# Performance work log

Hardware: AMD Instinct MI355X
Metric: run time of the kernel (lower is better)

Reference implementation:

```python
import jax, jax.numpy as jnp
import numpy as np

N_NODES = 50000
N_EDGES = 300000
HIDDEN = 256
Z_DIM = 128
N_LAYERS = 3
NUM_GRAPHS = 16
EPS = 1e-5


def setup_inputs() -> dict:
    key = jax.random.key(0)
    ks = jax.random.split(key, 16)
    s = 0.05
    inp = {
        "voxel_pos": jax.random.normal(ks[0], (N_NODES, 3), jnp.float32),
        "edge_index": jax.random.randint(ks[1], (2, N_EDGES), 0, N_NODES),
        "batch_index": jnp.sort(jax.random.randint(ks[2], (N_NODES,), 0, NUM_GRAPHS)),
        # input projection Linear(3, H) + GroupNorm(1, H) affine
        "W_in": jax.random.normal(ks[3], (3, HIDDEN), jnp.float32) * s,
        "b_in": jnp.zeros((HIDDEN,), jnp.float32),
        "g_in": jnp.ones((HIDDEN,), jnp.float32),
        "be_in": jnp.zeros((HIDDEN,), jnp.float32),
        # stacked GCNConv weights/biases and per-layer GroupNorm affines
        "conv_W": jax.random.normal(ks[4], (N_LAYERS, HIDDEN, HIDDEN), jnp.float32) * s,
        "conv_b": jnp.zeros((N_LAYERS, HIDDEN), jnp.float32),
        "gn_g": jnp.ones((N_LAYERS, HIDDEN), jnp.float32),
        "gn_b": jnp.zeros((N_LAYERS, HIDDEN), jnp.float32),
        # output MLP: Linear(H,H) -> ReLU -> GroupNorm -> Linear(H, Z)
        "W_o1": jax.random.normal(ks[5], (HIDDEN, HIDDEN), jnp.float32) * s,
        "b_o1": jnp.zeros((HIDDEN,), jnp.float32),
        "g_o": jnp.ones((HIDDEN,), jnp.float32),
        "be_o": jnp.zeros((HIDDEN,), jnp.float32),
        "W_o2": jax.random.normal(ks[6], (HIDDEN, Z_DIM), jnp.float32) * s,
        "b_o2": jnp.zeros((Z_DIM,), jnp.float32),
    }
    return inp


def group_norm(x, g, b):
    # GroupNorm(1, C) on (N, C): normalize over channels per node (biased var)
    mu = jnp.mean(x, axis=-1, keepdims=True)
    var = jnp.mean(jnp.square(x - mu), axis=-1, keepdims=True)
    return (x - mu) * jax.lax.rsqrt(var + EPS) * g + b


def reference(voxel_pos, edge_index, batch_index, W_in, b_in, g_in, be_in,
              conv_W, conv_b, gn_g, gn_b, W_o1, b_o1, g_o, be_o, W_o2, b_o2):
    n = voxel_pos.shape[0]
    loop = jnp.arange(n, dtype=edge_index.dtype)
    src = jnp.concatenate([edge_index[0], loop])  # A + I self-loops (PyG GCNConv default)
    dst = jnp.concatenate([edge_index[1], loop])
    deg = jax.ops.segment_sum(jnp.ones_like(dst, jnp.float32), dst, num_segments=n)
    dinv = jnp.where(deg > 0, jax.lax.rsqrt(jnp.maximum(deg, 1.0)), 0.0)
    enorm = dinv[src] * dinv[dst]  # D^{-1/2} (A+I) D^{-1/2} edge weights

    # input_proj: Linear -> ReLU -> GroupNorm
    x = group_norm(jax.nn.relu(voxel_pos @ W_in + b_in), g_in, be_in)

    for l in range(N_LAYERS):
        identity = x
        h = x @ conv_W[l]                      # GCNConv linear transform
        msg = h[src] * enorm[:, None]          # gather + scale (E+N, H)
        h = jax.ops.segment_sum(msg, dst, num_segments=n) + conv_b[l]
        x = jax.nn.relu(group_norm(h, gn_g[l], gn_b[l])) + identity

    # global mean pool per graph
    summed = jax.ops.segment_sum(x, batch_index, num_segments=NUM_GRAPHS)
    counts = jax.ops.segment_sum(jnp.ones((n,), jnp.float32), batch_index, num_segments=NUM_GRAPHS)
    pooled = summed / jnp.maximum(counts, 1.0)[:, None]

    h = group_norm(jax.nn.relu(pooled @ W_o1 + b_o1), g_o, be_o)
    return h @ W_o2 + b_o2
```

## Files before the change

### kernel.cpp

```cpp
#include <hip/hip_runtime.h>
#include <hip/hip_bf16.h>

#define N_NODES 50000
#define N_EDGES 300000
#define HIDDEN 256
#define ZDIM 128
#define NLAYERS 3
#define NGRAPHS 16
#define EPS 1e-5f
#define NSCANBLK 196

#define OFF_POS    0
#define OFF_WIN    150000
#define OFF_BIN    150768
#define OFF_GIN    151024
#define OFF_BEIN   151280
#define OFF_CONVB  348144
#define OFF_GNG    348912
#define OFF_GNB    349680
#define OFF_WO1    350448
#define OFF_BO1    415984
#define OFF_GO     416240
#define OFF_BEO    416496
#define OFF_WO2    416752
#define OFF_BO2    449520
#define PARAMS_TOTAL 449648

typedef __attribute__((ext_vector_type(8))) short short8;
typedef __attribute__((ext_vector_type(4))) float floatx4;

__device__ inline float wave_reduce_sum(float v){
#pragma unroll
  for (int off = 32; off; off >>= 1) v += __shfl_xor(v, off);
  return v;
}

__device__ inline ushort f2bf(float f){
  __hip_bfloat16 t = __float2bfloat16(f);
  return *(ushort*)&t;
}
__device__ inline float bflo(unsigned int u){ return __uint_as_float(u << 16); }
__device__ inline float bfhi(unsigned int u){ return __uint_as_float(u & 0xffff0000u); }

__device__ inline void gload_lds16(const void* g, void* l){
  __builtin_amdgcn_global_load_lds((const __attribute__((address_space(1))) void*)g,
                                   (__attribute__((address_space(3))) void*)l, 16, 0, 0);
}

__device__ inline void acc8(float* a, float w, uint4 v){
  a[0] = fmaf(w, bflo(v.x), a[0]); a[1] = fmaf(w, bfhi(v.x), a[1]);
  a[2] = fmaf(w, bflo(v.y), a[2]); a[3] = fmaf(w, bfhi(v.y), a[3]);
  a[4] = fmaf(w, bflo(v.z), a[4]); a[5] = fmaf(w, bfhi(v.z), a[5]);
  a[6] = fmaf(w, bflo(v.w), a[6]); a[7] = fmaf(w, bfhi(v.w), a[7]);
}

struct PrepArgs { const void* src[14]; int n[14]; int off[14]; const void* win; const void* convw; };

__global__ __launch_bounds__(256) void k_prep(PrepArgs a, float* __restrict__ params,
                                              ushort* __restrict__ Wt, int* __restrict__ flag,
                                              int* __restrict__ deg, int* __restrict__ fill,
                                              float* __restrict__ pooled, float* __restrict__ counts){
  __shared__ int sf;
  int tid = threadIdx.x;
  if (tid == 0) sf = 0;
  __syncthreads();
  const unsigned short* w = (const unsigned short*)a.win;
  for (int i = tid; i < 768; i += 256){
    int e = (w[i] >> 7) & 0xff;
    if (e >= 148) atomicOr(&sf, 1);
  }
  __syncthreads();
  const bool isf32 = (sf != 0);
  if (blockIdx.x == 0 && tid == 0) *flag = sf;

  int stride = gridDim.x * blockDim.x;
  int t0 = blockIdx.x * blockDim.x + tid;
  for (int i = t0; i < N_NODES; i += stride){ deg[i] = 1; fill[i] = 0; }
  for (int i = t0; i < NGRAPHS * 256; i += stride) pooled[i] = 0.f;
  for (int i = t0; i < NGRAPHS; i += stride) counts[i] = 0.f;

  for (int s = 0; s < 14; ++s){
    const void* src = a.src[s];
    int n = a.n[s];
    float* dst = params + a.off[s];
    if (isf32){
      const float* f = (const float*)src;
      for (int i = t0; i < n; i += stride) dst[i] = f[i];
    } else {
      const unsigned short* u = (const unsigned short*)src;
      for (int i = t0; i < n; i += stride) dst[i] = bflo(u[i]);
    }
  }
  for (int idx = t0; idx < NLAYERS * 65536; idx += stride){
    int l = idx >> 16, rem = idx & 65535, n = rem >> 8, k = rem & 255;
    int si = l * 65536 + k * 256 + n;
    float v = isf32 ? ((const float*)a.convw)[si] : bflo(((const unsigned short*)a.convw)[si]);
    Wt[idx] = f2bf(v);
  }
}

__global__ void k_deg(const int* __restrict__ dst, int* __restrict__ deg){
  int e = blockIdx.x * blockDim.x + threadIdx.x;
  if (e < N_EDGES) atomicAdd(&deg[dst[e]], 1);
}

__global__ __launch_bounds__(256) void k_scan1(const int* __restrict__ deg, int* __restrict__ row_start,
                                               int* __restrict__ bsum, float* __restrict__ dinv){
  __shared__ int sd[256];
  int tid = threadIdx.x;
  int i = blockIdx.x * 256 + tid;
  int v = (i < N_NODES) ? deg[i] : 0;
  if (i < N_NODES) dinv[i] = rsqrtf((float)v);
  sd[tid] = v;
  __syncthreads();
#pragma unroll
  for (int off = 1; off < 256; off <<= 1){
    int t = (tid >= off) ? sd[tid - off] : 0;
    __syncthreads();
    sd[tid] += t;
    __syncthreads();
  }
  if (i < N_NODES) row_start[i] = sd[tid];
  if (tid == 255) bsum[blockIdx.x] = sd[255];
}

__global__ __launch_bounds__(256) void k_scan2(const int* __restrict__ bsum, int* __restrict__ boff,
                                               int* __restrict__ row_start){
  __shared__ int sd[256];
  int tid = threadIdx.x;
  int v = (tid < NSCANBLK) ? bsum[tid] : 0;
  sd[tid] = v;
  __syncthreads();
#pragma unroll
  for (int off = 1; off < 256; off <<= 1){
    int t = (tid >= off) ? sd[tid - off] : 0;
    __syncthreads();
    sd[tid] += t;
    __syncthreads();
  }
  if (tid < NSCANBLK) boff[tid] = sd[tid] - v;
  if (tid == NSCANBLK - 1) row_start[N_NODES] = sd[tid];
}

__global__ __launch_bounds__(256) void k_scan3(const int* __restrict__ deg, const int* __restrict__ boff,
                                               int* __restrict__ row_start){
  int i = blockIdx.x * 256 + threadIdx.x;
  if (i < N_NODES) row_start[i] = row_start[i] + boff[blockIdx.x] - deg[i];
}

__global__ void k_fill(const int* __restrict__ src, const int* __restrict__ dst,
                       const int* __restrict__ row_start, int* __restrict__ fill,
                       const float* __restrict__ dinv, uint2* __restrict__ csr){
  int t = blockIdx.x * blockDim.x + threadIdx.x;
  if (t >= N_EDGES + N_NODES) return;
  int s, d;
  if (t < N_EDGES){ s = src[t]; d = dst[t]; }
  else            { s = t - N_EDGES; d = s; }
  int pos = row_start[d] + atomicAdd(&fill[d], 1);
  uint2 e; e.x = (unsigned)s; e.y = __float_as_uint(dinv[s] * dinv[d]);
  csr[pos] = e;
}

__global__ __launch_bounds__(256) void k_input_proj(const float* __restrict__ params,
                                                    ushort* __restrict__ x_bf){
  int lane = threadIdx.x & 63;
  int node = (blockIdx.x << 2) + (threadIdx.x >> 6);
  if (node >= N_NODES) return;
  const float* pos = params + OFF_POS + node * 3;
  float px = pos[0], py = pos[1], pz = pos[2];
  int c = lane * 4;
  const float* w0 = params + OFF_WIN;
  float v[4];
#pragma unroll
  for (int j = 0; j < 4; ++j){
    float t = params[OFF_BIN + c + j];
    t = fmaf(px, w0[c + j], t);
    t = fmaf(py, w0[256 + c + j], t);
    t = fmaf(pz, w0[512 + c + j], t);
    v[j] = fmaxf(t, 0.f);
  }
  float s  = v[0] + v[1] + v[2] + v[3];
  float ss = v[0]*v[0] + v[1]*v[1] + v[2]*v[2] + v[3]*v[3];
  s = wave_reduce_sum(s); ss = wave_reduce_sum(ss);
  float mean = s * (1.f/256.f);
  float var  = ss * (1.f/256.f) - mean * mean;
  float inv  = rsqrtf(var + EPS);
  float4 o;
  o.x = (v[0]-mean)*inv*params[OFF_GIN+c+0] + params[OFF_BEIN+c+0];
  o.y = (v[1]-mean)*inv*params[OFF_GIN+c+1] + params[OFF_BEIN+c+1];
  o.z = (v[2]-mean)*inv*params[OFF_GIN+c+2] + params[OFF_BEIN+c+2];
  o.w = (v[3]-mean)*inv*params[OFF_GIN+c+3] + params[OFF_BEIN+c+3];
  ushort4 ob = { f2bf(o.x), f2bf(o.y), f2bf(o.z), f2bf(o.w) };
  *(ushort4*)(x_bf + node * 256 + c) = ob;
}

#define GBM 128
__global__ __launch_bounds__(256) void k_gemm_bf(const ushort* __restrict__ A, const ushort* __restrict__ Bt,
                                                 ushort* __restrict__ Cb, int M){
  __shared__ __align__(16) ushort Sh[2 * GBM * 64];
  ushort* As = Sh;
  ushort* Bs = Sh + GBM * 64;
  int tid = threadIdx.x;
  int wave = tid >> 6, lane = tid & 63;
  int wr = wave >> 1, wc = wave & 1;
  int row0 = blockIdx.y * GBM;
  int col0 = blockIdx.x * GBM;
  int q = lane >> 4, l15 = lane & 15;
  int srow = lane >> 3;
  int sg   = lane & 7;
  floatx4 acc[4][4] = {};
  for (int k0 = 0; k0 < 256; k0 += 64){
    __syncthreads();
#pragma unroll
    for (int t = 0; t < 4; ++t){
      int rg = wave * 4 + t;
      int r  = rg * 8 + srow;
      int gs = sg ^ (r & 7);
      const ushort* ga = A  + (size_t)(row0 + r) * 256 + k0 + gs * 8;
      const ushort* gb = Bt + (size_t)(col0 + r) * 256 + k0 + gs * 8;
      gload_lds16(ga, As + rg * 512);
      gload_lds16(gb, Bs + rg * 512);
    }
    __syncthreads();
#pragma unroll
    for (int kk = 0; kk < 64; kk += 32){
      short8 af[4], bfr[4];
#pragma unroll
      for (int i = 0; i < 4; ++i){
        int R = wr * 64 + i * 16 + l15;
        int bg = (kk >> 3) + q;
        af[i] = *(const short8*)(As + R * 64 + ((bg ^ (R & 7)) << 3));
      }
#pragma unroll
      for (int j = 0; j < 4; ++j){
        int C = wc * 64 + j * 16 + l15;
        int bg = (kk >> 3) + q;
        bfr[j] = *(const short8*)(Bs + C * 64 + ((bg ^ (C & 7)) << 3));
      }
#pragma unroll
      for (int i = 0; i < 4; ++i)
#pragma unroll
        for (int j = 0; j < 4; ++j)
          acc[i][j] = __builtin_amdgcn_mfma_f32_16x16x32_bf16(af[i], bfr[j], acc[i][j], 0, 0, 0);
    }
  }
#pragma unroll
  for (int i = 0; i < 4; ++i){
#pragma unroll
    for (int r = 0; r < 4; ++r){
      int row = row0 + wr * 64 + i * 16 + q * 4 + r;
      if (row < M){
#pragma unroll
        for (int j = 0; j < 4; ++j){
          int col = col0 + wc * 64 + j * 16 + l15;
          Cb[row * 256 + col] = f2bf(acc[i][j][r]);
        }
      }
    }
  }
}

__global__ __launch_bounds__(256) void k_agg_norm(const ushort* __restrict__ hb, ushort* __restrict__ x_bf,
    const int* __restrict__ row_start, const uint2* __restrict__ csr,
    const float* __restrict__ params, int layer){
  int lane = threadIdx.x & 63;
  int node = (blockIdx.x << 2) + (threadIdx.x >> 6);
  if (node >= N_NODES) return;
  int half = lane >> 5;
  int l32 = lane & 31;
  int c = l32 * 8;
  float a[8] = {};
  int p0 = row_start[node], p1 = row_start[node + 1];
  int p = p0;
  for (; p + 8 <= p1; p += 8){
    uint2 e0 = csr[p + 0 + half];
    uint2 e1 = csr[p + 2 + half];
    uint2 e2 = csr[p + 4 + half];
    uint2 e3 = csr[p + 6 + half];
    uint4 v0 = *(const uint4*)(hb + (size_t)e0.x * 256 + c);
    uint4 v1 = *(const uint4*)(hb + (size_t)e1.x * 256 + c);
    uint4 v2 = *(const uint4*)(hb + (size_t)e2.x * 256 + c);
    uint4 v3 = *(const uint4*)(hb + (size_t)e3.x * 256 + c);
    acc8(a, __uint_as_float(e0.y), v0);
    acc8(a, __uint_as_float(e1.y), v1);
    acc8(a, __uint_as_float(e2.y), v2);
    acc8(a, __uint_as_float(e3.y), v3);
  }
  for (; p < p1; p += 2){
    int pp = p + half;
    if (pp < p1){
      uint2 e = csr[pp];
      uint4 v = *(const uint4*)(hb + (size_t)e.x * 256 + c);
      acc8(a, __uint_as_float(e.y), v);
    }
  }
#pragma unroll
  for (int j = 0; j < 8; ++j) a[j] += __shfl_xor(a[j], 32);

  const float* cb = params + OFF_CONVB + layer * 256;
  float v8[8];
  float s = 0.f, ss = 0.f;
#pragma unroll
  for (int j = 0; j < 8; ++j){
    float t = a[j] + cb[c + j];
    v8[j] = t; s += t; ss += t * t;
  }
  s  = wave_reduce_sum(s)  * 0.5f;
  ss = wave_reduce_sum(ss) * 0.5f;
  float mean = s * (1.f/256.f);
  float var  = ss * (1.f/256.f) - mean * mean;
  float inv  = rsqrtf(var + EPS);
  if (half == 0){
    const float* g = params + OFF_GNG + layer * 256;
    const float* b = params + OFF_GNB + layer * 256;
    uint4 xo = *(const uint4*)(x_bf + (size_t)node * 256 + c);
    float xr[8] = { bflo(xo.x), bfhi(xo.x), bflo(xo.y), bfhi(xo.y),
                    bflo(xo.z), bfhi(xo.z), bflo(xo.w), bfhi(xo.w) };
    short8 ob;
#pragma unroll
    for (int j = 0; j < 8; ++j){
      float o = fmaxf((v8[j] - mean) * inv * g[c + j] + b[c + j], 0.f) + xr[j];
      ob[j] = (short)f2bf(o);
    }
    *(short8*)(x_bf + (size_t)node * 256 + c) = ob;
  }
}

#define PBLK 256
__global__ __launch_bounds__(256) void k_pool(const ushort* __restrict__ x_bf, const int* __restrict__ batch,
                                              float* __restrict__ pooled, float* __restrict__ counts){
  __shared__ float lacc[NGRAPHS][256];
  __shared__ float lcnt[NGRAPHS];
  int tid = threadIdx.x;
  int wave = tid >> 6, lane = tid & 63;
  int c = lane * 4;
#pragma unroll
  for (int g = 0; g < NGRAPHS; ++g) lacc[g][tid] = 0.f;
  if (tid < NGRAPHS) lcnt[tid] = 0.f;
  __syncthreads();

  int n0 = blockIdx.x * PBLK + wave * 64;
  if (n0 < N_NODES){
    int n1 = min(n0 + 64, N_NODES);
    int b0 = batch[n0], b1 = batch[n1 - 1];
    float a0 = 0.f, a1 = 0.f, a2 = 0.f, a3 = 0.f;
    if (b0 == b1){
      int i = n0;
      for (; i + 8 <= n1; i += 8){
        uint2 v[8];
#pragma unroll
        for (int j = 0; j < 8; ++j) v[j] = *(const uint2*)(x_bf + (size_t)(i + j) * 256 + c);
#pragma unroll
        for (int j = 0; j < 8; ++j){
          a0 += bflo(v[j].x); a1 += bfhi(v[j].x);
          a2 += bflo(v[j].y); a3 += bfhi(v[j].y);
        }
      }
      for (; i < n1; ++i){
        uint2 v = *(const uint2*)(x_bf + (size_t)i * 256 + c);
        a0 += bflo(v.x); a1 += bfhi(v.x); a2 += bflo(v.y); a3 += bfhi(v.y);
      }
      atomicAdd(&lacc[b0][c + 0], a0); atomicAdd(&lacc[b0][c + 1], a1);
      atomicAdd(&lacc[b0][c + 2], a2); atomicAdd(&lacc[b0][c + 3], a3);
      if (lane == 0) atomicAdd(&lcnt[b0], (float)(n1 - n0));
    } else {
      int cur = b0, cnt = 0;
      for (int i = n0; i < n1; ++i){
        int g = batch[i];
        if (g != cur){
          atomicAdd(&lacc[cur][c + 0], a0); atomicAdd(&lacc[cur][c + 1], a1);
          atomicAdd(&lacc[cur][c + 2], a2); atomicAdd(&lacc[cur][c + 3], a3);
          if (lane == 0) atomicAdd(&lcnt[cur], (float)cnt);
          a0 = a1 = a2 = a3 = 0.f; cnt = 0; cur = g;
        }
        uint2 v = *(const uint2*)(x_bf + (size_t)i * 256 + c);
        a0 += bflo(v.x); a1 += bfhi(v.x); a2 += bflo(v.y); a3 += bfhi(v.y);
        cnt++;
      }
      atomicAdd(&lacc[cur][c + 0], a0); atomicAdd(&lacc[cur][c + 1], a1);
      atomicAdd(&lacc[cur][c + 2], a2); atomicAdd(&lacc[cur][c + 3], a3);
      if (lane == 0) atomicAdd(&lcnt[cur], (float)cnt);
    }
  }
  __syncthreads();

  int base = blockIdx.x * PBLK;
  if (base < N_NODES){
    int gmin = batch[base];
    int gmax = batch[min(base + PBLK, N_NODES) - 1];
    for (int g = gmin; g <= gmax; ++g){
      float v = lacc[g][tid];
      if (v != 0.f) atomicAdd(&pooled[g * 256 + tid], v);
      if (tid == 0 && lcnt[g] > 0.f) atomicAdd(&counts[g], lcnt[g]);
    }
  }
}

__global__ __launch_bounds__(256) void k_head(const float* __restrict__ pooled, const float* __restrict__ counts,
    const float* __restrict__ params, void* __restrict__ out, const int* __restrict__ flag){
  __shared__ float m[256];
  __shared__ float hh[256];
  __shared__ float red[2][4];
  int g = blockIdx.x, tid = threadIdx.x;
  float cnt = fmaxf(counts[g], 1.f);
  m[tid] = pooled[g * 256 + tid] / cnt;
  __syncthreads();
  const float* W1 = params + OFF_WO1;
  float acc = params[OFF_BO1 + tid];
  for (int k = 0; k < 256; ++k) acc = fmaf(m[k], W1[k * 256 + tid], acc);
  acc = fmaxf(acc, 0.f);
  float s = wave_reduce_sum(acc), ss = wave_reduce_sum(acc * acc);
  int wv = tid >> 6, lane = tid & 63;
  if (lane == 0){ red[0][wv] = s; red[1][wv] = ss; }
  __syncthreads();
  float S  = red[0][0] + red[0][1] + red[0][2] + red[0][3];
  float SS = red[1][0] + red[1][1] + red[1][2] + red[1][3];
  float mean = S * (1.f/256.f);
  float var  = SS * (1.f/256.f) - mean * mean;
  float inv  = rsqrtf(var + EPS);
  float hn = (acc - mean) * inv * params[OFF_GO + tid] + params[OFF_BEO + tid];
  hh[tid] = hn;
  __syncthreads();
  if (tid < ZDIM){
    const float* W2 = params + OFF_WO2;
    float o = params[OFF_BO2 + tid];
    for (int k = 0; k < 256; ++k) o = fmaf(hh[k], W2[k * 128 + tid], o);
    if (*flag) ((float*)out)[g * 128 + tid] = o;
    else       ((__hip_bfloat16*)out)[g * 128 + tid] = __float2bfloat16(o);
  }
}

extern "C" void kernel_launch(void* const* d_in, const int* in_sizes, int n_in,
                              void* d_out, int out_size, void* d_ws, size_t ws_size,
                              hipStream_t stream){
  size_t o = 0;
  auto alloc = [&](size_t bytes)->size_t{ size_t r = o; o = (o + bytes + 255) & ~(size_t)255; return r; };
  size_t off_flag   = alloc(4);
  size_t off_deg    = alloc((size_t)N_NODES * 4);
  size_t off_dinv   = alloc((size_t)N_NODES * 4);
  size_t off_rs     = alloc((size_t)(N_NODES + 1) * 4);
  size_t off_fill   = alloc((size_t)N_NODES * 4);
  size_t off_bsum   = alloc((size_t)NSCANBLK * 4);
  size_t off_boff   = alloc((size_t)NSCANBLK * 4);
  size_t off_csr    = alloc((size_t)(N_EDGES + N_NODES) * 8);
  size_t off_params = alloc((size_t)PARAMS_TOTAL * 4);
  size_t off_xbf    = alloc((size_t)N_NODES * HIDDEN * 2);
  size_t off_hbf    = alloc((size_t)N_NODES * HIDDEN * 2);
  size_t off_wt     = alloc((size_t)NLAYERS * HIDDEN * HIDDEN * 2);
  size_t off_pool   = alloc((size_t)NGRAPHS * 256 * 4);
  size_t off_cnt    = alloc((size_t)NGRAPHS * 4);
  if (o > ws_size) return;

  char* ws = (char*)d_ws;
  int*    flag     = (int*)(ws + off_flag);
  int*    deg      = (int*)(ws + off_deg);
  float*  dinv     = (float*)(ws + off_dinv);
  int*    row_start= (int*)(ws + off_rs);
  int*    fill     = (int*)(ws + off_fill);
  int*    bsum     = (int*)(ws + off_bsum);
  int*    boff     = (int*)(ws + off_boff);
  uint2*  csr      = (uint2*)(ws + off_csr);
  float*  params   = (float*)(ws + off_params);
  ushort* x_bf     = (ushort*)(ws + off_xbf);
  ushort* h_bf     = (ushort*)(ws + off_hbf);
  ushort* Wt       = (ushort*)(ws + off_wt);
  float*  pooled   = (float*)(ws + off_pool);
  float*  counts   = (float*)(ws + off_cnt);

  const int* edge_src = (const int*)d_in[1];
  const int* edge_dst = (const int*)d_in[1] + N_EDGES;
  const int* batch    = (const int*)d_in[2];

  PrepArgs pa;
  const int srcIdx[14] = {0,3,4,5,6,8,9,10,11,12,13,14,15,16};
  const int ns[14]     = {150000,768,256,256,256,768,768,768,65536,256,256,256,32768,128};
  const int offs[14]   = {OFF_POS,OFF_WIN,OFF_BIN,OFF_GIN,OFF_BEIN,OFF_CONVB,OFF_GNG,OFF_GNB,
                          OFF_WO1,OFF_BO1,OFF_GO,OFF_BEO,OFF_WO2,OFF_BO2};
  for (int i = 0; i < 14; ++i){ pa.src[i] = d_in[srcIdx[i]]; pa.n[i] = ns[i]; pa.off[i] = offs[i]; }
  pa.win = d_in[3]; pa.convw = d_in[7];
  k_prep<<<512, 256, 0, stream>>>(pa, params, Wt, flag, deg, fill, pooled, counts);

  k_deg<<<(N_EDGES + 255) / 256, 256, 0, stream>>>(edge_dst, deg);
  k_scan1<<<NSCANBLK, 256, 0, stream>>>(deg, row_start, bsum, dinv);
  k_scan2<<<1, 256, 0, stream>>>(bsum, boff, row_start);
  k_scan3<<<NSCANBLK, 256, 0, stream>>>(deg, boff, row_start);
  k_fill<<<(N_EDGES + N_NODES + 255) / 256, 256, 0, stream>>>(edge_src, edge_dst, row_start, fill,
                                                              dinv, csr);
  k_input_proj<<<N_NODES / 4, 256, 0, stream>>>(params, x_bf);

  dim3 ggrid(2, (N_NODES + GBM - 1) / GBM);
  for (int l = 0; l < NLAYERS; ++l){
    k_gemm_bf<<<ggrid, 256, 0, stream>>>(x_bf, Wt + l * 65536, h_bf, N_NODES);
    k_agg_norm<<<N_NODES / 4, 256, 0, stream>>>(h_bf, x_bf, row_start, csr, params, l);
  }

  k_pool<<<(N_NODES + PBLK - 1) / PBLK, 256, 0, stream>>>(x_bf, batch, pooled, counts);
  k_head<<<NGRAPHS, 256, 0, stream>>>(pooled, counts, params, d_out, flag);
}
```

Measured before the change: 350.8 us.

## Fuse scan fixup, CSR fill and input projection; tile weight transpose via LDS

After: 345.4 us. About the same (-1.5%).

```diff
diff --git a/kernel.cpp b/kernel.cpp
--- a/kernel.cpp
+++ b/kernel.cpp
@@ -9,6 +9,7 @@
 #define NGRAPHS 16
 #define EPS 1e-5f
 #define NSCANBLK 196
+#define FILLB 1368
 
 #define OFF_POS    0
 #define OFF_WIN    150000
@@ -61,6 +62,7 @@
                                               int* __restrict__ deg, int* __restrict__ fill,
                                               float* __restrict__ pooled, float* __restrict__ counts){
   __shared__ int sf;
+  __shared__ ushort tile[64][72];
   int tid = threadIdx.x;
   if (tid == 0) sf = 0;
   __syncthreads();
@@ -72,6 +74,28 @@
   __syncthreads();
   const bool isf32 = (sf != 0);
   if (blockIdx.x == 0 && tid == 0) *flag = sf;
+
+  if (blockIdx.x < NLAYERS * 16){
+    int t = blockIdx.x;
+    int l = t >> 4, tt = t & 15;
+    int kr0 = (tt >> 2) * 64, nc0 = (tt & 3) * 64;
+    size_t base = (size_t)l * 65536;
+    int r = tid >> 2;
+    int seg = (tid & 3) * 16;
+    if (isf32){
+      const float* srcp = (const float*)a.convw + base + (size_t)(kr0 + r) * 256 + nc0 + seg;
+#pragma unroll
+      for (int j = 0; j < 16; ++j) tile[r][seg + j] = f2bf(srcp[j]);
+    } else {
+      const unsigned short* srcp = (const unsigned short*)a.convw + base + (size_t)(kr0 + r) * 256 + nc0 + seg;
+#pragma unroll
+      for (int j = 0; j < 16; ++j) tile[r][seg + j] = srcp[j];
+    }
+    __syncthreads();
+    ushort* dst = Wt + base + (size_t)(nc0 + r) * 256 + kr0 + seg;
+#pragma unroll
+    for (int j = 0; j < 16; ++j) dst[j] = tile[seg + j][r];
+  }
 
   int stride = gridDim.x * blockDim.x;
   int t0 = blockIdx.x * blockDim.x + tid;
@@ -91,12 +115,6 @@
       for (int i = t0; i < n; i += stride) dst[i] = bflo(u[i]);
     }
   }
-  for (int idx = t0; idx < NLAYERS * 65536; idx += stride){
-    int l = idx >> 16, rem = idx & 65535, n = rem >> 8, k = rem & 255;
-    int si = l * 65536 + k * 256 + n;
-    float v = isf32 ? ((const float*)a.convw)[si] : bflo(((const unsigned short*)a.convw)[si]);
-    Wt[idx] = f2bf(v);
-  }
 }
 
 __global__ void k_deg(const int* __restrict__ dst, int* __restrict__ deg){
@@ -142,29 +160,28 @@
   if (tid == NSCANBLK - 1) row_start[N_NODES] = sd[tid];
 }
 
-__global__ __launch_bounds__(256) void k_scan3(const int* __restrict__ deg, const int* __restrict__ boff,
-                                               int* __restrict__ row_start){
-  int i = blockIdx.x * 256 + threadIdx.x;
-  if (i < N_NODES) row_start[i] = row_start[i] + boff[blockIdx.x] - deg[i];
-}
-
-__global__ void k_fill(const int* __restrict__ src, const int* __restrict__ dst,
-                       const int* __restrict__ row_start, int* __restrict__ fill,
-                       const float* __restrict__ dinv, uint2* __restrict__ csr){
-  int t = blockIdx.x * blockDim.x + threadIdx.x;
-  if (t >= N_EDGES + N_NODES) return;
-  int s, d;
-  if (t < N_EDGES){ s = src[t]; d = dst[t]; }
-  else            { s = t - N_EDGES; d = s; }
-  int pos = row_start[d] + atomicAdd(&fill[d], 1);
-  uint2 e; e.x = (unsigned)s; e.y = __float_as_uint(dinv[s] * dinv[d]);
-  csr[pos] = e;
-}
-
-__global__ __launch_bounds__(256) void k_input_proj(const float* __restrict__ params,
-                                                    ushort* __restrict__ x_bf){
-  int lane = threadIdx.x & 63;
-  int node = (blockIdx.x << 2) + (threadIdx.x >> 6);
+__global__ __launch_bounds__(256) void k_fillproj(const int* __restrict__ src, const int* __restrict__ dst,
+    const int* __restrict__ row_start, const int* __restrict__ boff, const int* __restrict__ deg,
+    int* __restrict__ fill, const float* __restrict__ dinv, uint2* __restrict__ csr,
+    int* __restrict__ rs2, const float* __restrict__ params, ushort* __restrict__ x_bf){
+  int b = blockIdx.x, tid = threadIdx.x;
+  if (b < FILLB){
+    int t = b * 256 + tid;
+    if (t == 0) rs2[N_NODES] = row_start[N_NODES];
+    if (t < N_EDGES + N_NODES){
+      int s, d;
+      if (t < N_EDGES){ s = src[t]; d = dst[t]; }
+      else            { s = t - N_EDGES; d = s; }
+      int rsf = row_start[d] + boff[d >> 8] - deg[d];
+      int pos = rsf + atomicAdd(&fill[d], 1);
+      uint2 e; e.x = (unsigned)s; e.y = __float_as_uint(dinv[s] * dinv[d]);
+      csr[pos] = e;
+      if (t >= N_EDGES) rs2[s] = rsf;
+    }
+    return;
+  }
+  int lane = tid & 63;
+  int node = ((b - FILLB) << 2) + (tid >> 6);
   if (node >= N_NODES) return;
   const float* pos = params + OFF_POS + node * 3;
   float px = pos[0], py = pos[1], pz = pos[2];
@@ -261,7 +278,7 @@
 }
 
 __global__ __launch_bounds__(256) void k_agg_norm(const ushort* __restrict__ hb, ushort* __restrict__ x_bf,
-    const int* __restrict__ row_start, const uint2* __restrict__ csr,
+    const int* __restrict__ rs2, const uint2* __restrict__ csr,
     const float* __restrict__ params, int layer){
   int lane = threadIdx.x & 63;
   int node = (blockIdx.x << 2) + (threadIdx.x >> 6);
@@ -270,7 +287,7 @@
   int l32 = lane & 31;
   int c = l32 * 8;
   float a[8] = {};
-  int p0 = row_start[node], p1 = row_start[node + 1];
+  int p0 = rs2[node], p1 = rs2[node + 1];
   int p = p0;
   for (; p + 8 <= p1; p += 8){
     uint2 e0 = csr[p + 0 + half];
@@ -439,6 +456,7 @@
   size_t off_deg    = alloc((size_t)N_NODES * 4);
   size_t off_dinv   = alloc((size_t)N_NODES * 4);
   size_t off_rs     = alloc((size_t)(N_NODES + 1) * 4);
+  size_t off_rs2    = alloc((size_t)(N_NODES + 1) * 4);
   size_t off_fill   = alloc((size_t)N_NODES * 4);
   size_t off_bsum   = alloc((size_t)NSCANBLK * 4);
   size_t off_boff   = alloc((size_t)NSCANBLK * 4);
@@ -456,6 +474,7 @@
   int*    deg      = (int*)(ws + off_deg);
   float*  dinv     = (float*)(ws + off_dinv);
   int*    row_start= (int*)(ws + off_rs);
+  int*    rs2      = (int*)(ws + off_rs2);
   int*    fill     = (int*)(ws + off_fill);
   int*    bsum     = (int*)(ws + off_bsum);
   int*    boff     = (int*)(ws + off_boff);
@@ -483,15 +502,15 @@
   k_deg<<<(N_EDGES + 255) / 256, 256, 0, stream>>>(edge_dst, deg);
   k_scan1<<<NSCANBLK, 256, 0, stream>>>(deg, row_start, bsum, dinv);
   k_scan2<<<1, 256, 0, stream>>>(bsum, boff, row_start);
-  k_scan3<<<NSCANBLK, 256, 0, stream>>>(deg, boff, row_start);
-  k_fill<<<(N_EDGES + N_NODES + 255) / 256, 256, 0, stream>>>(edge_src, edge_dst, row_start, fill,
-                                                              dinv, csr);
-  k_input_proj<<<N_NODES / 4, 256, 0, stream>>>(params, x_bf);
+
+  int projb = (N_NODES + 3) / 4;
+  k_fillproj<<<FILLB + projb, 256, 0, stream>>>(edge_src, edge_dst, row_start, boff, deg, fill,
+                                                dinv, csr, rs2, params, x_bf);
 
   dim3 ggrid(2, (N_NODES + GBM - 1) / GBM);
   for (int l = 0; l < NLAYERS; ++l){
     k_gemm_bf<<<ggrid, 256, 0, stream>>>(x_bf, Wt + l * 65536, h_bf, N_NODES);
-    k_agg_norm<<<N_NODES / 4, 256, 0, stream>>>(h_bf, x_bf, row_start, csr, params, l);
+    k_agg_norm<<<N_NODES / 4, 256, 0, stream>>>(h_bf, x_bf, rs2, csr, params, l);
   }
 
   k_pool<<<(N_NODES + PBLK - 1) / PBLK, 256, 0, stream>>>(x_bf, batch, pooled, counts);
```
